# Kernel tuning notes

Measured on AMD Instinct MI355X. Metric: run time of the kernel, lower is better.

## Reference

```python
import jax, jax.numpy as jnp
import numpy as np

DN = ('NCDHW', 'OIDHW', 'NCDHW')

def conv(x, w, stride=1):
    k = w.shape[-1]
    pad = 'VALID' if k == 2 else 'SAME'  # ks=2,s=2 Minkowski offsets {0,1}; ks=3 centered; ks=1 pointwise
    return jax.lax.conv_general_dilated(x, w, (stride,) * 3, pad, dimension_numbers=DN)

def masked_bn(x, m, eps=1e-5):
    # BatchNorm over occupied voxels only (MinkowskiBatchNorm semantics); affine is identity at init.
    cnt = jnp.maximum(jnp.sum(m), 1.0)
    mean = jnp.sum(x * m, axis=(0, 2, 3, 4)) / cnt
    xc = (x - mean.reshape(1, -1, 1, 1, 1)) * m  # also zeroes unoccupied sites
    var = jnp.sum(xc * xc, axis=(0, 2, 3, 4)) / cnt
    return xc * jax.lax.rsqrt(var + eps).reshape(1, -1, 1, 1, 1)

def downmask(m):
    B, _, D, H, W = m.shape
    return m.reshape(B, 1, D // 2, 2, H // 2, 2, W // 2, 2).max(axis=(3, 5, 7))

def cbr(x, m, w):
    return jax.nn.relu(masked_bn(conv(x, w), m))

def res(x, m, wa, wb, wsk):
    y = masked_bn(conv(jax.nn.relu(masked_bn(conv(x, wa), m)), wb), m)
    sk = x if wsk is None else masked_bn(conv(x, wsk), m)
    return jax.nn.relu(y + sk)

def stage(x, m, wd, wa1, wb1, wsk, wa2, wb2):
    m2 = downmask(m)  # output coord set of ks=2,s=2 sparse conv
    x = jax.nn.relu(masked_bn(conv(x, wd, 2), m2))  # BasicConvolutionBlock
    x = res(x, m2, wa1, wb1, wsk)
    x = res(x, m2, wa2, wb2, None)
    return x, m2

def _forward(feats, mask, ws0, ws1, d1, a11, b11, a12, b12, d2, a21, b21, k2, a22, b22,
             d3, a31, b31, k3, a32, b32, d4, a41, b41, k4, a42, b42):
    m = mask
    x = cbr(feats * m, m, ws0)
    x = cbr(x, m, ws1)
    x, m = stage(x, m, d1, a11, b11, None, a12, b12)   # 32 -> 32 (identity skip)
    x, m = stage(x, m, d2, a21, b21, k2, a22, b22)     # 32 -> 64
    x, m = stage(x, m, d3, a31, b31, k3, a32, b32)     # 64 -> 128
    x, m = stage(x, m, d4, a41, b41, k4, a42, b42)     # 128 -> 256
    return x

def setup_inputs() -> dict:
    key = jax.random.key(0)
    ks = jax.random.split(key, 28)
    def W(k, o, i, s):
        return jax.random.normal(k, (o, i, s, s, s), jnp.float32) / np.sqrt(i * s ** 3)
    feats = jax.random.normal(ks[0], (2, 3, 64, 64, 64), jnp.float32)
    mask = (jax.random.uniform(ks[1], (2, 1, 64, 64, 64)) < 0.1).astype(jnp.float32)
    return dict(
        feats=feats * mask, mask=mask,
        ws0=W(ks[2], 32, 3, 3), ws1=W(ks[3], 32, 32, 3),
        d1=W(ks[4], 32, 32, 2), a11=W(ks[5], 32, 32, 3), b11=W(ks[6], 32, 32, 3),
        a12=W(ks[7], 32, 32, 3), b12=W(ks[8], 32, 32, 3),
        d2=W(ks[9], 32, 32, 2), a21=W(ks[10], 64, 32, 3), b21=W(ks[11], 64, 64, 3),
        k2=W(ks[12], 64, 32, 1), a22=W(ks[13], 64, 64, 3), b22=W(ks[14], 64, 64, 3),
        d3=W(ks[15], 64, 64, 2), a31=W(ks[16], 128, 64, 3), b31=W(ks[17], 128, 128, 3),
        k3=W(ks[18], 128, 64, 1), a32=W(ks[19], 128, 128, 3), b32=W(ks[20], 128, 128, 3),
        d4=W(ks[21], 128, 128, 2), a41=W(ks[22], 256, 128, 3), b41=W(ks[23], 256, 256, 3),
        k4=W(ks[24], 256, 128, 1), a42=W(ks[25], 256, 256, 3), b42=W(ks[26], 256, 256, 3))

def reference(feats, mask, ws0, ws1, d1, a11, b11, a12, b12, d2, a21, b21, k2, a22, b22,
              d3, a31, b31, k3, a32, b32, d4, a41, b41, k4, a42, b42):
    return _forward(feats, mask, ws0, ws1, d1, a11, b11, a12, b12, d2, a21, b21, k2, a22, b22,
                    d3, a31, b31, k3, a32, b32, d4, a41, b41, k4, a42, b42)
```

## Files before the change

kernel.cpp:

```cpp
#include <hip/hip_runtime.h>

#define BLK 256

static inline int gup(long work) { return (int)((work + BLK - 1) / BLK); }

__device__ inline bool occ_pred(const float* mask, const int* fmap,
                                int i, int DHW, int Ho, int Wo, int mode) {
  if (mode == 0) return mask[i] > 0.f;
  int b = i / DHW, sp = i - b * DHW;
  int HW = Ho * Wo;
  int z = sp / HW, r = sp - z * HW, y = r / Wo, x = r - y * Wo;
  int Hi = 2 * Ho, Wi = 2 * Wo;
  const int* mb = fmap + b * 8 * DHW;
  int base = ((2 * z) * Hi + 2 * y) * Wi + 2 * x;
  bool occ = false;
  for (int dz = 0; dz < 2; dz++)
    for (int dy = 0; dy < 2; dy++)
      for (int dx = 0; dx < 2; dx++)
        occ |= mb[base + dz * Hi * Wi + dy * Wi + dx] >= 0;
  return occ;
}

__global__ __launch_bounds__(1024) void cnt_k(const float* mask, const int* fmap,
    int* bcnt, int DHW, int Ho, int Wo, int mode, int total) {
  int i = blockIdx.x * 1024 + threadIdx.x;
  bool occ = (i < total) && occ_pred(mask, fmap, i, DHW, Ho, Wo, mode);
  unsigned long long bal = __ballot(occ);
  __shared__ int ws[16];
  int lane = threadIdx.x & 63, wid = threadIdx.x >> 6;
  if (lane == 0) ws[wid] = __popcll(bal);
  __syncthreads();
  if (threadIdx.x == 0) {
    int a = 0;
    for (int w = 0; w < 16; w++) a += ws[w];
    bcnt[blockIdx.x] = a;
  }
}

__global__ __launch_bounds__(1024) void scan_k(int* bcnt, int nb, int* cnt) {
  __shared__ int sh[1024];
  int t = threadIdx.x;
  int v = (t < nb) ? bcnt[t] : 0;
  sh[t] = v;
  __syncthreads();
  for (int o = 1; o < 1024; o <<= 1) {
    int u = (t >= o) ? sh[t - o] : 0;
    __syncthreads();
    sh[t] += u;
    __syncthreads();
  }
  if (t < nb) bcnt[t] = sh[t] - v;
  if (t == 0) *cnt = sh[1023];
}

__global__ __launch_bounds__(1024) void emit_k(const float* mask, const int* fmap,
    const int* boff, int* map, int* list, int DHW, int Ho, int Wo, int mode, int total) {
  int i = blockIdx.x * 1024 + threadIdx.x;
  bool occ = (i < total) && occ_pred(mask, fmap, i, DHW, Ho, Wo, mode);
  unsigned long long bal = __ballot(occ);
  int lane = threadIdx.x & 63, wid = threadIdx.x >> 6;
  __shared__ int wcnt[16], woff[16];
  if (lane == 0) wcnt[wid] = __popcll(bal);
  __syncthreads();
  if (threadIdx.x == 0) {
    int a = boff[blockIdx.x];
    for (int w = 0; w < 16; w++) { woff[w] = a; a += wcnt[w]; }
  }
  __syncthreads();
  if (i < total) {
    if (occ) {
      int p = woff[wid] + __popcll(bal & ((1ull << lane) - 1ull));
      map[i] = p; list[p] = i;
    } else map[i] = -1;
  }
}

__global__ __launch_bounds__(1024) void compact1_k(const int* __restrict__ fmap,
    int* __restrict__ map, int* __restrict__ list, int* __restrict__ cntp,
    int Do, int Ho, int Wo) {
  int DHW = Do * Ho * Wo, total = 2 * DHW;
  int tid = threadIdx.x, lane = tid & 63, wid = tid >> 6;
  bool occ = (tid < total) && occ_pred(nullptr, fmap, tid, DHW, Ho, Wo, 1);
  unsigned long long bal = __ballot(occ);
  __shared__ int wcnt[16], woff[16];
  if (lane == 0) wcnt[wid] = __popcll(bal);
  __syncthreads();
  if (tid == 0) {
    int a = 0;
    for (int w = 0; w < 16; w++) { woff[w] = a; a += wcnt[w]; }
    *cntp = a;
  }
  __syncthreads();
  if (tid < total) {
    if (occ) {
      int p = woff[wid] + __popcll(bal & ((1ull << lane) - 1ull));
      map[tid] = p; list[p] = tid;
    } else map[tid] = -1;
  }
}

__global__ __launch_bounds__(256) void csr_both_k(
    const int* __restrict__ list, const int* __restrict__ map,
    const int* __restrict__ cntp, const int* __restrict__ fmap,
    int* __restrict__ csr27, int* __restrict__ csr8,
    int D, int H, int W, int do8) {
  int n = *cntp;
  int DHW = D * H * W;
  for (int v = blockIdx.x * 256 + threadIdx.x; v < n; v += gridDim.x * 256) {
    int idx = list[v];
    int b = idx / DHW, sp = idx - b * DHW;
    int z = sp / (H * W), r = sp - z * H * W, y = r / W, x = r - y * W;
    const int* mb = map + b * DHW;
    int* e = csr27 + (long)v * 28;
    int cnt = 0;
    for (int k = 0; k < 27; k++) {
      int dz = k / 9 - 1, dy = (k / 3) % 3 - 1, dx = k % 3 - 1;
      int zz = z + dz, yy = y + dy, xx = x + dx;
      if ((unsigned)zz >= (unsigned)D || (unsigned)yy >= (unsigned)H ||
          (unsigned)xx >= (unsigned)W) continue;
      int j = mb[(zz * H + yy) * W + xx];
      if (j >= 0) e[++cnt] = (k << 24) | j;
    }
    e[0] = cnt;
    for (int s = cnt + 1; s <= 27; s++) e[s] = -1;
    if (do8) {
      int Hi = 2 * H, Wi = 2 * W;
      const int* fb = fmap + b * 8 * DHW;
      int* e8 = csr8 + (long)v * 9;
      int c8 = 0;
      for (int k = 0; k < 8; k++) {
        int dz = k >> 2, dy = (k >> 1) & 1, dx = k & 1;
        int j = fb[((2 * z + dz) * Hi + 2 * y + dy) * Wi + 2 * x + dx];
        if (j >= 0) e8[++c8] = (k << 24) | j;
      }
      e8[0] = c8;
      for (int s = c8 + 1; s <= 8; s++) e8[s] = -1;
    }
  }
}

struct WAll {
  const float* src[25];
  float* dst[25];
  int O[25], I[25], K[25];
  int sb[26];
};

__global__ __launch_bounds__(256) void wtr_all_k(WAll wa) {
  int b = blockIdx.x;
  int w = 0;
  while (w < 24 && b >= wa.sb[w + 1]) ++w;
  int O = wa.O[w], I = wa.I[w], K = wa.K[w];
  int I4 = (I + 3) >> 2;
  long tot = (long)K * I4 * O * 4;
  long t = (long)(b - wa.sb[w]) * 256 + threadIdx.x;
  if (t >= tot) return;
  int e = (int)(t & 3); long r = t >> 2;
  int co = (int)(r % O); long r2 = r / O;
  int ci4 = (int)(r2 % I4); int k = (int)(r2 / I4);
  int ci = 4 * ci4 + e;
  wa.dst[w][t] = (ci < I) ? wa.src[w][((long)co * I + ci) * K + k] : 0.f;
}

__global__ void gather0_k(const float* __restrict__ feats, const int* __restrict__ list,
                          const int* __restrict__ cntp, float* __restrict__ rows, int DHW) {
  int n = *cntp;
  int t = blockIdx.x * BLK + threadIdx.x;
  if (t >= n * 4) return;
  int vox = t >> 2, c = t & 3;
  int idx = list[vox]; int b = idx / DHW, sp = idx - b * DHW;
  rows[t] = (c < 3) ? feats[(b * 3 + c) * DHW + sp] : 0.f;
}

template <int CIN, int COUT, int CPT, int VX, int NT, int TG, bool PRE>
__global__ __launch_bounds__(256) void convk_k(
    const float* __restrict__ fin, const float* __restrict__ wt,
    float* __restrict__ fout, const int* __restrict__ csr,
    const int* __restrict__ cntp, const int* __restrict__ pcntp,
    const float* __restrict__ pslot, float* __restrict__ slot) {
  constexpr int CL = COUT / CPT;
  constexpr int G = 256 / CL;
  constexpr int VT = G * VX;
  constexpr int C4 = CIN / 4;
  constexpr int RST = C4 + 1;
  constexpr int WSZ = C4 * COUT;
  __shared__ int jtab[VT * NT];
  __shared__ float4 rbuf[VT * RST];
  __shared__ float4 wbuf[WSZ];
  __shared__ float aP[PRE ? CIN : 4], bP[PRE ? CIN : 4];
  __shared__ float swA[256], swB[256];
  int n = *cntp;
  int vb = blockIdx.x * VT;
  if (vb >= n) return;
  int tid = threadIdx.x;
  if constexpr (PRE) {
    int np = *pcntp;
    float c = fmaxf((float)np, 1.f);
    for (int ch = tid; ch < CIN; ch += 256) {
      float s = 0.f, q = 0.f;
      #pragma unroll
      for (int r = 0; r < 4; r++) { s += pslot[r * 512 + ch]; q += pslot[r * 512 + 256 + ch]; }
      float mean = s / c, var = fmaxf(q / c - mean * mean, 0.f);
      float a = rsqrtf(var + 1e-5f);
      aP[ch] = a; bP[ch] = -mean * a;
    }
  }
  for (int u = tid; u < VT * NT; u += 256) jtab[u] = -1;
  __syncthreads();
  for (int u = tid; u < VT * (NT + 1); u += 256) {
    int v = u / (NT + 1), s = u - v * (NT + 1);
    if (s > 0 && vb + v < n) {
      int e = csr[(long)(vb + v) * (NT + 1) + s];
      if (e >= 0) jtab[v * NT + (e >> 24)] = e & 0xFFFFFF;
    }
  }
  int cl = tid % CL, g = tid / CL;
  float acc[VX][CPT];
  #pragma unroll
  for (int vx = 0; vx < VX; vx++)
    #pragma unroll
    for (int m = 0; m < CPT; m++) acc[vx][m] = 0.f;
  const float4* fin4 = (const float4*)fin;
  const float4* w4 = (const float4*)wt;
  const int tg0 = (TG > 1) ? (int)blockIdx.y : 0;
  for (int k = tg0; k < NT; k += TG) {
    __syncthreads();
    for (int u = tid; u < WSZ; u += 256) wbuf[u] = w4[(long)k * WSZ + u];
    for (int u = tid; u < VT * C4; u += 256) {
      int v = u / C4, c4 = u - v * C4;
      int j = jtab[v * NT + k];
      float4 val = make_float4(0.f, 0.f, 0.f, 0.f);
      if (j >= 0) {
        val = fin4[(long)j * C4 + c4];
        if constexpr (PRE) {
          int ch = 4 * c4;
          val.x = fmaxf(val.x * aP[ch] + bP[ch], 0.f);
          val.y = fmaxf(val.y * aP[ch + 1] + bP[ch + 1], 0.f);
          val.z = fmaxf(val.z * aP[ch + 2] + bP[ch + 2], 0.f);
          val.w = fmaxf(val.w * aP[ch + 3] + bP[ch + 3], 0.f);
        }
      }
      rbuf[v * RST + c4] = val;
    }
    __syncthreads();
    #pragma unroll
    for (int c4 = 0; c4 < C4; c4++) {
      float4 w_[CPT];
      #pragma unroll
      for (int m = 0; m < CPT; m++) w_[m] = wbuf[c4 * COUT + cl + m * CL];
      #pragma unroll
      for (int vx = 0; vx < VX; vx++) {
        float4 rv = rbuf[(g + vx * G) * RST + c4];
        #pragma unroll
        for (int m = 0; m < CPT; m++)
          acc[vx][m] += rv.x * w_[m].x + rv.y * w_[m].y + rv.z * w_[m].z + rv.w * w_[m].w;
      }
    }
  }
  #pragma unroll
  for (int vx = 0; vx < VX; vx++) {
    int v = vb + g + vx * G;
    if (v < n) {
      #pragma unroll
      for (int m = 0; m < CPT; m++) {
        if constexpr (TG > 1)
          atomicAdd(&fout[(long)v * COUT + cl + m * CL], acc[vx][m]);
        else
          fout[(long)v * COUT + cl + m * CL] = acc[vx][m];
      }
    }
  }
  if constexpr (TG == 1) {
    int lane = tid & 63, wid = tid >> 6;
    bool alive[VX];
    #pragma unroll
    for (int vx = 0; vx < VX; vx++) alive[vx] = (vb + g + vx * G) < n;
    #pragma unroll
    for (int m = 0; m < CPT; m++) {
      float ps = 0.f, pq = 0.f;
      #pragma unroll
      for (int vx = 0; vx < VX; vx++)
        if (alive[vx]) { ps += acc[vx][m]; pq += acc[vx][m] * acc[vx][m]; }
      #pragma unroll
      for (int o = 32; o >= CL; o >>= 1) {
        ps += __shfl_down(ps, o);
        pq += __shfl_down(pq, o);
      }
      if (lane < CL) {
        swA[(m * 4 + wid) * CL + lane] = ps;
        swB[(m * 4 + wid) * CL + lane] = pq;
      }
    }
    __syncthreads();
    if (tid < COUT) {
      int m = tid / CL, c2 = tid % CL;
      float s = 0.f, q = 0.f;
      #pragma unroll
      for (int w = 0; w < 4; w++) {
        s += swA[(m * 4 + w) * CL + c2];
        q += swB[(m * 4 + w) * CL + c2];
      }
      float* sl = slot + (blockIdx.x & 3) * 512;
      atomicAdd(&sl[tid], s);
      atomicAdd(&sl[256 + tid], q);
    }
  }
}

template <int CIN, int COUT, int COT, int VT, int KSP, bool PRE>
__global__ __launch_bounds__(256) void convw_k(
    const float* __restrict__ fin, const float* __restrict__ wt,
    float* __restrict__ fout, const int* __restrict__ csr,
    const int* __restrict__ cntp, const int* __restrict__ pcntp,
    const float* __restrict__ pslot) {
  constexpr int CL = COT / 2;
  constexpr int G = 256 / CL;
  constexpr int VX = VT / G;
  constexpr int C4 = CIN / 4;
  constexpr int RST = C4 + 1;
  __shared__ float4 wbuf[C4 * COT];
  __shared__ float4 rbuf[VT * RST];
  __shared__ int jt[VT * 27];
  __shared__ int act[27];
  __shared__ float aP[PRE ? CIN : 4], bP[PRE ? CIN : 4];
  int n = *cntp;
  int vb = blockIdx.x * VT;
  if (vb >= n) return;
  int tid = threadIdx.x;
  int c0 = blockIdx.y * COT;
  if constexpr (PRE) {
    int np = *pcntp;
    float c = fmaxf((float)np, 1.f);
    for (int ch = tid; ch < CIN; ch += 256) {
      float s = 0.f, q = 0.f;
      #pragma unroll
      for (int r = 0; r < 4; r++) { s += pslot[r * 512 + ch]; q += pslot[r * 512 + 256 + ch]; }
      float mean = s / c, var = fmaxf(q / c - mean * mean, 0.f);
      float a = rsqrtf(var + 1e-5f);
      aP[ch] = a; bP[ch] = -mean * a;
    }
  }
  if (tid < 27) act[tid] = 0;
  for (int u = tid; u < VT * 27; u += 256) jt[u] = -1;
  __syncthreads();
  for (int u = tid; u < VT * 28; u += 256) {
    int v = u / 28, s = u - v * 28;
    if (s > 0 && vb + v < n) {
      int e = csr[(long)(vb + v) * 28 + s];
      if (e >= 0) {
        int k = e >> 24;
        jt[v * 27 + k] = e & 0xFFFFFF;
        atomicOr(&act[k], 1);
      }
    }
  }
  __syncthreads();
  int cl = tid % CL, g = tid / CL, vg = g * VX;
  float acc[VX][2];
  #pragma unroll
  for (int vx = 0; vx < VX; vx++) { acc[vx][0] = 0.f; acc[vx][1] = 0.f; }
  const float4* fin4 = (const float4*)fin;
  const float4* w4 = (const float4*)wt;
  for (int k = blockIdx.z; k < 27; k += KSP) {
    if (!act[k]) continue;
    __syncthreads();
    for (int u = tid; u < C4 * COT; u += 256) {
      int ci4 = u / COT, co = u - ci4 * COT;
      wbuf[u] = w4[(long)k * C4 * COUT + ci4 * COUT + c0 + co];
    }
    for (int u = tid; u < VT * C4; u += 256) {
      int v = u / C4, c4 = u - v * C4;
      int j = jt[v * 27 + k];
      float4 val = make_float4(0.f, 0.f, 0.f, 0.f);
      if (j >= 0) {
        val = fin4[(long)j * C4 + c4];
        if constexpr (PRE) {
          int ch = 4 * c4;
          val.x = fmaxf(val.x * aP[ch] + bP[ch], 0.f);
          val.y = fmaxf(val.y * aP[ch + 1] + bP[ch + 1], 0.f);
          val.z = fmaxf(val.z * aP[ch + 2] + bP[ch + 2], 0.f);
          val.w = fmaxf(val.w * aP[ch + 3] + bP[ch + 3], 0.f);
        }
      }
      rbuf[v * RST + c4] = val;
    }
    __syncthreads();
    #pragma unroll 8
    for (int c4 = 0; c4 < C4; c4++) {
      float4 w0 = wbuf[c4 * COT + cl];
      float4 w1 = wbuf[c4 * COT + cl + CL];
      #pragma unroll
      for (int vx = 0; vx < VX; vx++) {
        float4 rv = rbuf[(vg + vx) * RST + c4];
        acc[vx][0] += rv.x * w0.x + rv.y * w0.y + rv.z * w0.z + rv.w * w0.w;
        acc[vx][1] += rv.x * w1.x + rv.y * w1.y + rv.z * w1.z + rv.w * w1.w;
      }
    }
  }
  #pragma unroll
  for (int vx = 0; vx < VX; vx++) {
    int v = vb + vg + vx;
    if (v < n) {
      atomicAdd(&fout[(long)v * COUT + c0 + cl], acc[vx][0]);
      atomicAdd(&fout[(long)v * COUT + c0 + cl + CL], acc[vx][1]);
    }
  }
}

template <int CIN, int COUT, int ES, bool PRE>
__global__ __launch_bounds__(256) void convc_k(
    const float* __restrict__ fin, const float* __restrict__ wt,
    float* __restrict__ fout, const int* __restrict__ csr,
    const int* __restrict__ cntp, const int* __restrict__ pcntp,
    const float* __restrict__ pslot, float* __restrict__ slot) {
  constexpr int CL = COUT / 2, G = 256 / CL, C4 = CIN / 4;
  constexpr int EST = (ES > 0) ? ES : 1;
  constexpr int CPD = PRE ? CIN : 4;
  __shared__ float4 rbuf[G * C4];
  __shared__ int se[G * EST];
  __shared__ float aP[CPD], bP[CPD];
  __shared__ float sA[256], sB[256];
  __shared__ int scmax;
  int n = *cntp;
  int vb = blockIdx.x * G;
  if (vb >= n) return;
  int tid = threadIdx.x;
  if constexpr (PRE) {
    int np = *pcntp;
    float c = fmaxf((float)np, 1.f);
    for (int ch = tid; ch < CIN; ch += 256) {
      float s = 0.f, q = 0.f;
      #pragma unroll
      for (int r = 0; r < 4; r++) { s += pslot[r * 512 + ch]; q += pslot[r * 512 + 256 + ch]; }
      float mean = s / c, var = fmaxf(q / c - mean * mean, 0.f);
      float a = rsqrtf(var + 1e-5f);
      aP[ch] = a; bP[ch] = -mean * a;
    }
  }
  int cmax;
  if constexpr (ES > 0) {
    if (tid == 0) scmax = 0;
    __syncthreads();
    for (int u = tid; u < G * ES; u += 256) {
      int v = vb + u / ES;
      int e = (v < n) ? csr[(long)vb * ES + u] : 0;
      se[u] = e;
      if ((u % ES) == 0) atomicMax(&scmax, e);
    }
    __syncthreads();
    cmax = scmax;
  } else {
    __syncthreads();
    cmax = 1;
  }
  int cl = tid % CL, g = tid / CL;
  int v = vb + g;
  bool alive = v < n;
  float a0 = 0.f, a1 = 0.f;
  const float4* fin4 = (const float4*)fin;
  const float4* w4 = (const float4*)wt;
  for (int i = 1; i <= cmax; i++) {
    __syncthreads();
    for (int u = tid; u < G * C4; u += 256) {
      int gg = u / C4, c4 = u - gg * C4;
      int pj = -1;
      if constexpr (ES > 0) {
        if (vb + gg < n && i <= se[gg * EST]) pj = se[gg * EST + i];
      } else {
        if (vb + gg < n) pj = vb + gg;
      }
      float4 val = make_float4(0.f, 0.f, 0.f, 0.f);
      if (pj >= 0) {
        int j = pj & 0xFFFFFF;
        val = fin4[(long)j * C4 + c4];
        if constexpr (PRE) {
          int ch = 4 * c4;
          val.x = fmaxf(val.x * aP[ch] + bP[ch], 0.f);
          val.y = fmaxf(val.y * aP[ch + 1] + bP[ch + 1], 0.f);
          val.z = fmaxf(val.z * aP[ch + 2] + bP[ch + 2], 0.f);
          val.w = fmaxf(val.w * aP[ch + 3] + bP[ch + 3], 0.f);
        }
      }
      rbuf[u] = val;
    }
    __syncthreads();
    int pj;
    if constexpr (ES > 0) {
      pj = (alive && i <= se[g * EST]) ? se[g * EST + i] : -1;
    } else {
      pj = alive ? v : -1;
    }
    if (pj >= 0) {
      int k = pj >> 24;
      const float4* wk = w4 + (long)k * C4 * COUT + cl;
      #pragma unroll 8
      for (int c4 = 0; c4 < C4; c4++) {
        float4 rv = rbuf[g * C4 + c4];
        float4 w0 = wk[c4 * COUT];
        float4 w1 = wk[c4 * COUT + CL];
        a0 += rv.x * w0.x + rv.y * w0.y + rv.z * w0.z + rv.w * w0.w;
        a1 += rv.x * w1.x + rv.y * w1.y + rv.z * w1.z + rv.w * w1.w;
      }
    }
  }
  if (alive) {
    fout[(long)v * COUT + cl] = a0;
    fout[(long)v * COUT + cl + CL] = a1;
  }
  __syncthreads();
  sA[tid] = alive ? a0 : 0.f; sB[tid] = alive ? a1 : 0.f;
  __syncthreads();
  for (int o = 128; o >= CL; o >>= 1) {
    if (tid < o) { sA[tid] += sA[tid + o]; sB[tid] += sB[tid + o]; }
    __syncthreads();
  }
  float s0 = 0.f, s1 = 0.f;
  if (tid < CL) { s0 = sA[tid]; s1 = sB[tid]; }
  __syncthreads();
  sA[tid] = alive ? a0 * a0 : 0.f; sB[tid] = alive ? a1 * a1 : 0.f;
  __syncthreads();
  for (int o = 128; o >= CL; o >>= 1) {
    if (tid < o) { sA[tid] += sA[tid + o]; sB[tid] += sB[tid + o]; }
    __syncthreads();
  }
  if (tid < CL) {
    float* sl = slot + (blockIdx.x & 3) * 512;
    atomicAdd(&sl[tid], s0);
    atomicAdd(&sl[tid + CL], s1);
    atomicAdd(&sl[256 + tid], sA[tid]);
    atomicAdd(&sl[256 + tid + CL], sB[tid]);
  }
}

template <int C>
__global__ __launch_bounds__(BLK) void bnred_k(const float* __restrict__ rows,
    const int* __restrict__ cntp, float* __restrict__ slot) {
  int n = *cntp;
  long tot = (long)n * C;
  int tid = threadIdx.x;
  float s = 0.f, s2 = 0.f;
  for (long t = (long)blockIdx.x * BLK + tid; t < tot; t += (long)gridDim.x * BLK) {
    float v = rows[t]; s += v; s2 += v * v;
  }
  __shared__ float sh[BLK], sh2[BLK];
  sh[tid] = s; sh2[tid] = s2;
  __syncthreads();
  for (int o = BLK / 2; o >= C; o >>= 1) {
    if (tid < o) { sh[tid] += sh[tid + o]; sh2[tid] += sh2[tid + o]; }
    __syncthreads();
  }
  if (tid < C) { atomicAdd(&slot[tid], sh[tid]); atomicAdd(&slot[256 + tid], sh2[tid]); }
}

template <int C, int MODE>
__global__ __launch_bounds__(256) void skipapp_k(
    const float* __restrict__ x, const float* __restrict__ y,
    const float* __restrict__ s1, const float* __restrict__ s2,
    const int* __restrict__ cntp, float* __restrict__ out) {
  __shared__ float a1_[C], b1_[C], a2_[C], b2_[C];
  int n = *cntp;
  int tid = threadIdx.x;
  float cnt = fmaxf((float)n, 1.f);
  for (int c = tid; c < C; c += 256) {
    float s = 0.f, q = 0.f;
    #pragma unroll
    for (int r = 0; r < 4; r++) { s += s1[r * 512 + c]; q += s1[r * 512 + 256 + c]; }
    float mean = s / cnt, var = fmaxf(q / cnt - mean * mean, 0.f);
    float a = rsqrtf(var + 1e-5f);
    a1_[c] = a; b1_[c] = -mean * a;
    if (MODE != 2) {
      s = 0.f; q = 0.f;
      #pragma unroll
      for (int r = 0; r < 4; r++) { s += s2[r * 512 + c]; q += s2[r * 512 + 256 + c]; }
      mean = s / cnt; var = fmaxf(q / cnt - mean * mean, 0.f);
      a = rsqrtf(var + 1e-5f);
      a2_[c] = a; b2_[c] = -mean * a;
    }
  }
  __syncthreads();
  constexpr int C4 = C / 4;
  long tot = (long)n * C4;
  for (long t = (long)blockIdx.x * 256 + tid; t < tot; t += (long)gridDim.x * 256) {
    int c = 4 * (int)(t % C4);
    float4 xv = ((const float4*)x)[t];
    float4 yv = ((const float4*)y)[t];
    float4 o;
    o.x = xv.x * a1_[c] + b1_[c];
    o.y = xv.y * a1_[c + 1] + b1_[c + 1];
    o.z = xv.z * a1_[c + 2] + b1_[c + 2];
    o.w = xv.w * a1_[c + 3] + b1_[c + 3];
    if (MODE == 0) {
      o.x += yv.x * a2_[c] + b2_[c];
      o.y += yv.y * a2_[c + 1] + b2_[c + 1];
      o.z += yv.z * a2_[c + 2] + b2_[c + 2];
      o.w += yv.w * a2_[c + 3] + b2_[c + 3];
    } else if (MODE == 1) {
      o.x += fmaxf(yv.x * a2_[c] + b2_[c], 0.f);
      o.y += fmaxf(yv.y * a2_[c + 1] + b2_[c + 1], 0.f);
      o.z += fmaxf(yv.z * a2_[c + 2] + b2_[c + 2], 0.f);
      o.w += fmaxf(yv.w * a2_[c + 3] + b2_[c + 3], 0.f);
    } else {
      o.x += yv.x; o.y += yv.y; o.z += yv.z; o.w += yv.w;
    }
    o.x = fmaxf(o.x, 0.f); o.y = fmaxf(o.y, 0.f);
    o.z = fmaxf(o.z, 0.f); o.w = fmaxf(o.w, 0.f);
    ((float4*)out)[t] = o;
  }
}

__global__ void scatter_k(const float* __restrict__ rows, const int* __restrict__ list,
                          const int* __restrict__ cntp, float* __restrict__ out, int DHW) {
  int n = *cntp;
  int t = blockIdx.x * BLK + threadIdx.x;
  if (t >= n * 256) return;
  int vox = t >> 8, c = t & 255;
  int idx = list[vox]; int b = idx / DHW, sp = idx - b * DHW;
  out[(b * 256 + c) * DHW + sp] = rows[t];
}

#define CAP0 81920
#define CAP1 57344
#define CAP2 8192
#define CAP3 1024
#define CAP4 128

extern "C" void kernel_launch(void* const* d_in, const int* in_sizes, int n_in,
                              void* d_out, int out_size, void* d_ws, size_t ws_size,
                              hipStream_t stream) {
  const float* feats = (const float*)d_in[0];
  const float* mask0 = (const float*)d_in[1];

  char* p = (char*)d_ws;
  auto alloc = [&](size_t bytes) { char* r = p; p += (bytes + 255) & ~255ull; return r; };

  const int tab[25][4] = {
    {2, 32, 3, 27},  {3, 32, 32, 27}, {4, 32, 32, 8},  {5, 32, 32, 27}, {6, 32, 32, 27},
    {7, 32, 32, 27}, {8, 32, 32, 27}, {9, 32, 32, 8},  {10, 64, 32, 27},{11, 64, 64, 27},
    {12, 64, 32, 1}, {13, 64, 64, 27},{14, 64, 64, 27},{15, 64, 64, 8}, {16, 128, 64, 27},
    {17, 128, 128, 27},{18, 128, 64, 1},{19, 128, 128, 27},{20, 128, 128, 27},
    {21, 128, 128, 8},{22, 256, 128, 27},{23, 256, 256, 27},{24, 256, 128, 1},
    {25, 256, 256, 27},{26, 256, 256, 27},
  };
  WAll wa;
  float* wT[27] = {nullptr};
  int blk = 0;
  for (int i = 0; i < 25; i++) {
    int idx = tab[i][0], O = tab[i][1], I = tab[i][2], K = tab[i][3];
    int I4 = (I + 3) / 4;
    long sz = (long)K * I4 * O * 4;
    wT[idx] = (float*)alloc((size_t)sz * 4);
    wa.src[i] = (const float*)d_in[idx]; wa.dst[i] = wT[idx];
    wa.O[i] = O; wa.I[i] = I; wa.K[i] = K;
    wa.sb[i] = blk; blk += (int)((sz + 255) / 256);
  }
  wa.sb[25] = blk;

  int* map0 = (int*)alloc(524288 * 4);
  int* list0 = (int*)alloc((size_t)CAP0 * 4);
  int* map1 = (int*)alloc(65536 * 4);
  int* list1 = (int*)alloc((size_t)CAP1 * 4);
  int* map2 = (int*)alloc(8192 * 4);
  int* list2 = (int*)alloc(8192 * 4);
  int* map3 = (int*)alloc(1024 * 4);
  int* list3 = (int*)alloc(1024 * 4);
  int* map4 = (int*)alloc(128 * 4);
  int* list4 = (int*)alloc(128 * 4);
  int* bcnt = (int*)alloc(1024 * 4);
  int* cnts = (int*)alloc(32 * 4);
  int* c27_0 = (int*)alloc((size_t)CAP0 * 28 * 4);
  int* c27_1 = (int*)alloc((size_t)CAP1 * 28 * 4);
  int* c8_1  = (int*)alloc((size_t)CAP1 * 9 * 4);
  int* c27_2 = (int*)alloc((size_t)CAP2 * 28 * 4);
  int* c8_2  = (int*)alloc((size_t)CAP2 * 9 * 4);
  int* c27_3 = (int*)alloc((size_t)CAP3 * 28 * 4);
  int* c8_3  = (int*)alloc((size_t)CAP3 * 9 * 4);
  int* c27_4 = (int*)alloc((size_t)CAP4 * 28 * 4);
  int* c8_4  = (int*)alloc((size_t)CAP4 * 9 * 4);
  float* stats = (float*)alloc(25 * 2048 * 4);
  float* G0  = (float*)alloc((size_t)CAP0 * 4 * 4);
  float* F0a = (float*)alloc((size_t)CAP0 * 32 * 4);
  char* zstart = p;
  float* F0b = (float*)alloc((size_t)CAP0 * 32 * 4);
  float* R1[6];
  for (int i = 0; i < 6; i++) R1[i] = (float*)alloc((size_t)CAP1 * 32 * 4);
  float* R2[6];
  for (int i = 0; i < 6; i++) R2[i] = (float*)alloc((size_t)CAP2 * 64 * 4);
  size_t zlen = (size_t)(p - zstart);
  size_t z3sz = (size_t)CAP3 * 128 * 4 * 6 + (size_t)CAP4 * 256 * 4 * 6;
  float* Z3 = (float*)alloc(z3sz);
  float* R3[6], *R4[6];
  for (int i = 0; i < 6; i++) R3[i] = Z3 + (size_t)i * CAP3 * 128;
  for (int i = 0; i < 6; i++) R4[i] = Z3 + (size_t)6 * CAP3 * 128 + (size_t)i * CAP4 * 256;

  hipMemsetAsync(stats, 0, 25 * 2048 * 4, stream);
  hipMemsetAsync(zstart, 0, zlen, stream);
  hipMemsetAsync(Z3, 0, z3sz, stream);
  hipMemsetAsync(d_out, 0, (size_t)out_size * 4, stream);

  wtr_all_k<<<blk, 256, 0, stream>>>(wa);

  int* n0 = cnts + 0; int* n1 = cnts + 1; int* n2 = cnts + 2;
  int* n3 = cnts + 3; int* n4 = cnts + 4;

  cnt_k<<<512, 1024, 0, stream>>>(mask0, nullptr, bcnt, 262144, 64, 64, 0, 524288);
  scan_k<<<1, 1024, 0, stream>>>(bcnt, 512, n0);
  emit_k<<<512, 1024, 0, stream>>>(mask0, nullptr, bcnt, map0, list0, 262144, 64, 64, 0, 524288);
  gather0_k<<<gup((long)CAP0 * 4), BLK, 0, stream>>>(feats, list0, n0, G0, 262144);
  csr_both_k<<<512, 256, 0, stream>>>(list0, map0, n0, nullptr, c27_0, nullptr, 64, 64, 64, 0);

  cnt_k<<<64, 1024, 0, stream>>>(nullptr, map0, bcnt, 32768, 32, 32, 1, 65536);
  scan_k<<<1, 1024, 0, stream>>>(bcnt, 64, n1);
  emit_k<<<64, 1024, 0, stream>>>(nullptr, map0, bcnt, map1, list1, 32768, 32, 32, 1, 65536);
  csr_both_k<<<256, 256, 0, stream>>>(list1, map1, n1, map0, c27_1, c8_1, 32, 32, 32, 1);

  cnt_k<<<8, 1024, 0, stream>>>(nullptr, map1, bcnt, 4096, 16, 16, 1, 8192);
  scan_k<<<1, 1024, 0, stream>>>(bcnt, 8, n2);
  emit_k<<<8, 1024, 0, stream>>>(nullptr, map1, bcnt, map2, list2, 4096, 16, 16, 1, 8192);
  csr_both_k<<<32, 256, 0, stream>>>(list2, map2, n2, map1, c27_2, c8_2, 16, 16, 16, 1);

  compact1_k<<<1, 1024, 0, stream>>>(map2, map3, list3, n3, 8, 8, 8);
  csr_both_k<<<4, 256, 0, stream>>>(list3, map3, n3, map2, c27_3, c8_3, 8, 8, 8, 1);

  compact1_k<<<1, 1024, 0, stream>>>(map3, map4, list4, n4, 4, 4, 4);
  csr_both_k<<<1, 256, 0, stream>>>(list4, map4, n4, map3, c27_4, c8_4, 4, 4, 4, 1);

  auto slot = [&](int i) { return stats + (size_t)i * 2048; };
  auto bgrid = [&](long cap, int C) { long g = (cap * C / 4 + 255) / 256; return (int)(g > 2048 ? 2048 : g); };

  int rb0 = 512, rb1 = 512, rb2 = 512;

  {
    int g = CAP0 / 128;
    convk_k<4, 32, 4, 4, 27, 1, false><<<g, 256, 0, stream>>>(G0, wT[2], F0a, c27_0, n0, nullptr, nullptr, slot(0));
    convk_k<32, 32, 4, 4, 27, 2, true><<<dim3(g, 2), 256, 0, stream>>>(F0a, wT[3], F0b, c27_0, n0, n0, slot(0), nullptr);
    bnred_k<32><<<rb0, BLK, 0, stream>>>(F0b, n0, slot(1));
  }

  {
    int g = CAP1 / 128, ag = bgrid(CAP1, 32);
    convk_k<32, 32, 4, 4, 8, 2, true><<<dim3(g, 2), 256, 0, stream>>>(F0b, wT[4], R1[0], c8_1, n1, n0, slot(1), nullptr);
    bnred_k<32><<<rb1, BLK, 0, stream>>>(R1[0], n1, slot(2));
    convk_k<32, 32, 4, 4, 27, 2, true><<<dim3(g, 2), 256, 0, stream>>>(R1[0], wT[5], R1[1], c27_1, n1, n1, slot(2), nullptr);
    bnred_k<32><<<rb1, BLK, 0, stream>>>(R1[1], n1, slot(3));
    convk_k<32, 32, 4, 4, 27, 2, true><<<dim3(g, 2), 256, 0, stream>>>(R1[1], wT[6], R1[2], c27_1, n1, n1, slot(3), nullptr);
    bnred_k<32><<<rb1, BLK, 0, stream>>>(R1[2], n1, slot(4));
    skipapp_k<32, 1><<<ag, 256, 0, stream>>>(R1[2], R1[0], slot(4), slot(2), n1, R1[3]);
    convk_k<32, 32, 4, 4, 27, 2, false><<<dim3(g, 2), 256, 0, stream>>>(R1[3], wT[7], R1[4], c27_1, n1, nullptr, nullptr, nullptr);
    bnred_k<32><<<rb1, BLK, 0, stream>>>(R1[4], n1, slot(5));
    convk_k<32, 32, 4, 4, 27, 2, true><<<dim3(g, 2), 256, 0, stream>>>(R1[4], wT[8], R1[5], c27_1, n1, n1, slot(5), nullptr);
    bnred_k<32><<<rb1, BLK, 0, stream>>>(R1[5], n1, slot(6));
    skipapp_k<32, 2><<<ag, 256, 0, stream>>>(R1[5], R1[3], slot(6), nullptr, n1, R1[3]);
  }

  {
    int g64 = CAP2 / 64, ag = bgrid(CAP2, 64);
    convk_k<32, 32, 4, 2, 8, 2, false><<<dim3(g64 * 2, 2), 256, 0, stream>>>(R1[3], wT[9], R2[0], c8_2, n2, nullptr, nullptr, nullptr);
    bnred_k<32><<<rb2, BLK, 0, stream>>>(R2[0], n2, slot(7));
    convk_k<32, 64, 4, 4, 27, 4, true><<<dim3(g64, 4), 256, 0, stream>>>(R2[0], wT[10], R2[1], c27_2, n2, n2, slot(7), nullptr);
    bnred_k<64><<<rb2, BLK, 0, stream>>>(R2[1], n2, slot(8));
    convk_k<64, 64, 4, 4, 27, 4, true><<<dim3(g64, 4), 256, 0, stream>>>(R2[1], wT[11], R2[2], c27_2, n2, n2, slot(8), nullptr);
    bnred_k<64><<<rb2, BLK, 0, stream>>>(R2[2], n2, slot(9));
    convc_k<32, 64, 0, true><<<(CAP2 + 7) / 8, 256, 0, stream>>>(R2[0], wT[12], R2[3], nullptr, n2, n2, slot(7), slot(10));
    skipapp_k<64, 0><<<ag, 256, 0, stream>>>(R2[2], R2[3], slot(9), slot(10), n2, R2[3]);
    convk_k<64, 64, 4, 4, 27, 4, false><<<dim3(g64, 4), 256, 0, stream>>>(R2[3], wT[13], R2[4], c27_2, n2, nullptr, nullptr, nullptr);
    bnred_k<64><<<rb2, BLK, 0, stream>>>(R2[4], n2, slot(11));
    convk_k<64, 64, 4, 4, 27, 4, true><<<dim3(g64, 4), 256, 0, stream>>>(R2[4], wT[14], R2[5], c27_2, n2, n2, slot(11), nullptr);
    bnred_k<64><<<rb2, BLK, 0, stream>>>(R2[5], n2, slot(12));
    skipapp_k<64, 2><<<ag, 256, 0, stream>>>(R2[5], R2[3], slot(12), nullptr, n2, R2[3]);
  }

  {
    int gP = (CAP3 + 7) / 8, gO = (CAP3 + 3) / 4, ag = bgrid(CAP3, 128);
    int rO = gup((long)CAP3 * 128); if (rO > 512) rO = 512;
    dim3 gw(CAP3 / 16, 1, 4);
    convc_k<64, 64, 9, false><<<gP, 256, 0, stream>>>(R2[3], wT[15], R3[0], c8_3, n3, nullptr, nullptr, slot(13));
    convw_k<64, 128, 128, 16, 4, true><<<gw, 256, 0, stream>>>(R3[0], wT[16], R3[1], c27_3, n3, n3, slot(13));
    bnred_k<128><<<rO, BLK, 0, stream>>>(R3[1], n3, slot(14));
    convw_k<128, 128, 128, 16, 4, true><<<gw, 256, 0, stream>>>(R3[1], wT[17], R3[2], c27_3, n3, n3, slot(14));
    bnred_k<128><<<rO, BLK, 0, stream>>>(R3[2], n3, slot(15));
    convc_k<64, 128, 0, true><<<gO, 256, 0, stream>>>(R3[0], wT[18], R3[3], nullptr, n3, n3, slot(13), slot(16));
    skipapp_k<128, 0><<<ag, 256, 0, stream>>>(R3[2], R3[3], slot(15), slot(16), n3, R3[1]);
    convw_k<128, 128, 128, 16, 4, false><<<gw, 256, 0, stream>>>(R3[1], wT[19], R3[4], c27_3, n3, nullptr, nullptr);
    bnred_k<128><<<rO, BLK, 0, stream>>>(R3[4], n3, slot(17));
    convw_k<128, 128, 128, 16, 4, true><<<gw, 256, 0, stream>>>(R3[4], wT[20], R3[5], c27_3, n3, n3, slot(17));
    bnred_k<128><<<rO, BLK, 0, stream>>>(R3[5], n3, slot(18));
    skipapp_k<128, 2><<<ag, 256, 0, stream>>>(R3[5], R3[1], slot(18), nullptr, n3, R3[0]);
  }

  {
    int gP = (CAP4 + 3) / 4, gO = (CAP4 + 1) / 2, ag = bgrid(CAP4, 256);
    int rO = gup((long)CAP4 * 256); if (rO > 512) rO = 512;
    dim3 gw(CAP4 / 16, 4, 8);
    convc_k<128, 128, 9, false><<<gP, 256, 0, stream>>>(R3[0], wT[21], R4[0], c8_4, n4, nullptr, nullptr, slot(19));
    convw_k<128, 256, 64, 16, 8, true><<<gw, 256, 0, stream>>>(R4[0], wT[22], R4[1], c27_4, n4, n4, slot(19));
    bnred_k<256><<<rO, BLK, 0, stream>>>(R4[1], n4, slot(20));
    convw_k<256, 256, 64, 16, 8, true><<<gw, 256, 0, stream>>>(R4[1], wT[23], R4[2], c27_4, n4, n4, slot(20));
    bnred_k<256><<<rO, BLK, 0, stream>>>(R4[2], n4, slot(21));
    convc_k<128, 256, 0, true><<<gO, 256, 0, stream>>>(R4[0], wT[24], R4[3], nullptr, n4, n4, slot(19), slot(22));
    skipapp_k<256, 0><<<ag, 256, 0, stream>>>(R4[2], R4[3], slot(21), slot(22), n4, R4[1]);
    convw_k<256, 256, 64, 16, 8, false><<<gw, 256, 0, stream>>>(R4[1], wT[25], R4[4], c27_4, n4, nullptr, nullptr);
    bnred_k<256><<<rO, BLK, 0, stream>>>(R4[4], n4, slot(23));
    convw_k<256, 256, 64, 16, 8, true><<<gw, 256, 0, stream>>>(R4[4], wT[26], R4[5], c27_4, n4, n4, slot(23));
    bnred_k<256><<<rO, BLK, 0, stream>>>(R4[5], n4, slot(24));
    skipapp_k<256, 2><<<ag, 256, 0, stream>>>(R4[5], R4[1], slot(24), nullptr, n4, R4[0]);
  }

  scatter_k<<<gup((long)CAP4 * 256), BLK, 0, stream>>>(R4[0], list4, n4, (float*)d_out, 64);
}
```

Baseline: 1.649 ms.

## Retile sparse conv kernels and fuse BN stats into stage-0/1 convs

Measured after the change: 2.043 ms. 1.24x slower.

```diff
diff --git a/kernel.cpp b/kernel.cpp
--- a/kernel.cpp
+++ b/kernel.cpp
@@ -188,7 +188,7 @@
   __shared__ float4 rbuf[VT * RST];
   __shared__ float4 wbuf[WSZ];
   __shared__ float aP[PRE ? CIN : 4], bP[PRE ? CIN : 4];
-  __shared__ float swA[256], swB[256];
+  __shared__ float swA[CPT * 4 * CL], swB[CPT * 4 * CL];
   int n = *cntp;
   int vb = blockIdx.x * VT;
   if (vb >= n) return;
@@ -245,15 +245,15 @@
     __syncthreads();
     #pragma unroll
     for (int c4 = 0; c4 < C4; c4++) {
-      float4 w_[CPT];
-      #pragma unroll
-      for (int m = 0; m < CPT; m++) w_[m] = wbuf[c4 * COUT + cl + m * CL];
-      #pragma unroll
-      for (int vx = 0; vx < VX; vx++) {
-        float4 rv = rbuf[(g + vx * G) * RST + c4];
+      float4 rv[VX];
+      #pragma unroll
+      for (int vx = 0; vx < VX; vx++) rv[vx] = rbuf[(g + vx * G) * RST + c4];
+      #pragma unroll
+      for (int m = 0; m < CPT; m++) {
+        float4 w = wbuf[c4 * COUT + cl + m * CL];
         #pragma unroll
-        for (int m = 0; m < CPT; m++)
-          acc[vx][m] += rv.x * w_[m].x + rv.y * w_[m].y + rv.z * w_[m].z + rv.w * w_[m].w;
+        for (int vx = 0; vx < VX; vx++)
+          acc[vx][m] += rv[vx].x * w.x + rv[vx].y * w.y + rv[vx].z * w.z + rv[vx].w * w.w;
       }
     }
   }
@@ -679,10 +679,10 @@
   float* stats = (float*)alloc(25 * 2048 * 4);
   float* G0  = (float*)alloc((size_t)CAP0 * 4 * 4);
   float* F0a = (float*)alloc((size_t)CAP0 * 32 * 4);
-  char* zstart = p;
   float* F0b = (float*)alloc((size_t)CAP0 * 32 * 4);
   float* R1[6];
   for (int i = 0; i < 6; i++) R1[i] = (float*)alloc((size_t)CAP1 * 32 * 4);
+  char* zstart = p;
   float* R2[6];
   for (int i = 0; i < 6; i++) R2[i] = (float*)alloc((size_t)CAP2 * 64 * 4);
   size_t zlen = (size_t)(p - zstart);
@@ -727,44 +727,39 @@
   auto slot = [&](int i) { return stats + (size_t)i * 2048; };
   auto bgrid = [&](long cap, int C) { long g = (cap * C / 4 + 255) / 256; return (int)(g > 2048 ? 2048 : g); };
 
-  int rb0 = 512, rb1 = 512, rb2 = 512;
+  int g0 = CAP0 / 128;
+  int g1 = CAP1 / 128;
+  int rb2 = 512;
 
   {
-    int g = CAP0 / 128;
-    convk_k<4, 32, 4, 4, 27, 1, false><<<g, 256, 0, stream>>>(G0, wT[2], F0a, c27_0, n0, nullptr, nullptr, slot(0));
-    convk_k<32, 32, 4, 4, 27, 2, true><<<dim3(g, 2), 256, 0, stream>>>(F0a, wT[3], F0b, c27_0, n0, n0, slot(0), nullptr);
-    bnred_k<32><<<rb0, BLK, 0, stream>>>(F0b, n0, slot(1));
+    convk_k<4, 32, 16, 1, 27, 1, false><<<g0, 256, 0, stream>>>(G0, wT[2], F0a, c27_0, n0, nullptr, nullptr, slot(0));
+    convk_k<32, 32, 16, 1, 27, 1, true><<<g0, 256, 0, stream>>>(F0a, wT[3], F0b, c27_0, n0, n0, slot(0), slot(1));
   }
 
   {
-    int g = CAP1 / 128, ag = bgrid(CAP1, 32);
-    convk_k<32, 32, 4, 4, 8, 2, true><<<dim3(g, 2), 256, 0, stream>>>(F0b, wT[4], R1[0], c8_1, n1, n0, slot(1), nullptr);
-    bnred_k<32><<<rb1, BLK, 0, stream>>>(R1[0], n1, slot(2));
-    convk_k<32, 32, 4, 4, 27, 2, true><<<dim3(g, 2), 256, 0, stream>>>(R1[0], wT[5], R1[1], c27_1, n1, n1, slot(2), nullptr);
-    bnred_k<32><<<rb1, BLK, 0, stream>>>(R1[1], n1, slot(3));
-    convk_k<32, 32, 4, 4, 27, 2, true><<<dim3(g, 2), 256, 0, stream>>>(R1[1], wT[6], R1[2], c27_1, n1, n1, slot(3), nullptr);
-    bnred_k<32><<<rb1, BLK, 0, stream>>>(R1[2], n1, slot(4));
+    int ag = bgrid(CAP1, 32);
+    convk_k<32, 32, 16, 1, 8, 1, true><<<g1, 256, 0, stream>>>(F0b, wT[4], R1[0], c8_1, n1, n0, slot(1), slot(2));
+    convk_k<32, 32, 16, 1, 27, 1, true><<<g1, 256, 0, stream>>>(R1[0], wT[5], R1[1], c27_1, n1, n1, slot(2), slot(3));
+    convk_k<32, 32, 16, 1, 27, 1, true><<<g1, 256, 0, stream>>>(R1[1], wT[6], R1[2], c27_1, n1, n1, slot(3), slot(4));
     skipapp_k<32, 1><<<ag, 256, 0, stream>>>(R1[2], R1[0], slot(4), slot(2), n1, R1[3]);
-    convk_k<32, 32, 4, 4, 27, 2, false><<<dim3(g, 2), 256, 0, stream>>>(R1[3], wT[7], R1[4], c27_1, n1, nullptr, nullptr, nullptr);
-    bnred_k<32><<<rb1, BLK, 0, stream>>>(R1[4], n1, slot(5));
-    convk_k<32, 32, 4, 4, 27, 2, true><<<dim3(g, 2), 256, 0, stream>>>(R1[4], wT[8], R1[5], c27_1, n1, n1, slot(5), nullptr);
-    bnred_k<32><<<rb1, BLK, 0, stream>>>(R1[5], n1, slot(6));
+    convk_k<32, 32, 16, 1, 27, 1, false><<<g1, 256, 0, stream>>>(R1[3], wT[7], R1[4], c27_1, n1, nullptr, nullptr, slot(5));
+    convk_k<32, 32, 16, 1, 27, 1, true><<<g1, 256, 0, stream>>>(R1[4], wT[8], R1[5], c27_1, n1, n1, slot(5), slot(6));
     skipapp_k<32, 2><<<ag, 256, 0, stream>>>(R1[5], R1[3], slot(6), nullptr, n1, R1[3]);
   }
 
   {
-    int g64 = CAP2 / 64, ag = bgrid(CAP2, 64);
-    convk_k<32, 32, 4, 2, 8, 2, false><<<dim3(g64 * 2, 2), 256, 0, stream>>>(R1[3], wT[9], R2[0], c8_2, n2, nullptr, nullptr, nullptr);
+    int ag = bgrid(CAP2, 64);
+    convk_k<32, 32, 16, 1, 8, 2, false><<<dim3(64, 2), 256, 0, stream>>>(R1[3], wT[9], R2[0], c8_2, n2, nullptr, nullptr, nullptr);
     bnred_k<32><<<rb2, BLK, 0, stream>>>(R2[0], n2, slot(7));
-    convk_k<32, 64, 4, 4, 27, 4, true><<<dim3(g64, 4), 256, 0, stream>>>(R2[0], wT[10], R2[1], c27_2, n2, n2, slot(7), nullptr);
+    convk_k<32, 64, 16, 2, 27, 4, true><<<dim3(64, 4), 256, 0, stream>>>(R2[0], wT[10], R2[1], c27_2, n2, n2, slot(7), nullptr);
     bnred_k<64><<<rb2, BLK, 0, stream>>>(R2[1], n2, slot(8));
-    convk_k<64, 64, 4, 4, 27, 4, true><<<dim3(g64, 4), 256, 0, stream>>>(R2[1], wT[11], R2[2], c27_2, n2, n2, slot(8), nullptr);
+    convk_k<64, 64, 16, 2, 27, 4, true><<<dim3(64, 4), 256, 0, stream>>>(R2[1], wT[11], R2[2], c27_2, n2, n2, slot(8), nullptr);
     bnred_k<64><<<rb2, BLK, 0, stream>>>(R2[2], n2, slot(9));
     convc_k<32, 64, 0, true><<<(CAP2 + 7) / 8, 256, 0, stream>>>(R2[0], wT[12], R2[3], nullptr, n2, n2, slot(7), slot(10));
     skipapp_k<64, 0><<<ag, 256, 0, stream>>>(R2[2], R2[3], slot(9), slot(10), n2, R2[3]);
-    convk_k<64, 64, 4, 4, 27, 4, false><<<dim3(g64, 4), 256, 0, stream>>>(R2[3], wT[13], R2[4], c27_2, n2, nullptr, nullptr, nullptr);
+    convk_k<64, 64, 16, 2, 27, 4, false><<<dim3(64, 4), 256, 0, stream>>>(R2[3], wT[13], R2[4], c27_2, n2, nullptr, nullptr, nullptr);
     bnred_k<64><<<rb2, BLK, 0, stream>>>(R2[4], n2, slot(11));
-    convk_k<64, 64, 4, 4, 27, 4, true><<<dim3(g64, 4), 256, 0, stream>>>(R2[4], wT[14], R2[5], c27_2, n2, n2, slot(11), nullptr);
+    convk_k<64, 64, 16, 2, 27, 4, true><<<dim3(64, 4), 256, 0, stream>>>(R2[4], wT[14], R2[5], c27_2, n2, n2, slot(11), nullptr);
     bnred_k<64><<<rb2, BLK, 0, stream>>>(R2[5], n2, slot(12));
     skipapp_k<64, 2><<<ag, 256, 0, stream>>>(R2[5], R2[3], slot(12), nullptr, n2, R2[3]);
   }
```
